# Kernel optimization log

Hardware: AMD Instinct MI355X
Metric: run time of the kernel (lower is better)

The kernel has to match this reference:

```python
import jax, jax.numpy as jnp
import numpy as np

N_NODES = 100000

def setup_inputs() -> dict:
    key = jax.random.key(0)
    ks = jax.random.split(key, 8)
    n_feat, nhid, nclass = 256, 128, 40
    n_edges = 1600000
    x = jax.random.normal(ks[0], (N_NODES, n_feat), dtype=jnp.float32)
    edge_index = jax.random.randint(ks[1], (2, n_edges), 0, N_NODES, dtype=jnp.int64)
    # Glorot-ish scaled weights
    W1 = jax.random.normal(ks[2], (n_feat, nhid), dtype=jnp.float32) / np.sqrt(n_feat)
    b1 = jnp.zeros((nhid,), dtype=jnp.float32)
    W2 = jax.random.normal(ks[3], (nhid, nhid), dtype=jnp.float32) / np.sqrt(nhid)
    b2 = jnp.zeros((nhid,), dtype=jnp.float32)
    Wc = jax.random.normal(ks[4], (nhid, nclass), dtype=jnp.float32) / np.sqrt(nhid)
    bc = jnp.zeros((nclass,), dtype=jnp.float32)
    return {"x": x, "edge_index": edge_index, "W1": W1, "b1": b1,
            "W2": W2, "b2": b2, "Wc": Wc, "bc": bc}


def _gcn_conv(x, src, dst, W, b, n_nodes):
    """PyG GCNConv: transform, then sym-normalized aggregation with self-loops.
    out_i = sum_{j in N(i) u {i}} (d_i^-1/2 d_j^-1/2) (x_j W) + b,
    where d = in-degree over A + I.
    """
    h = x @ W  # [N, out]
    ones = jnp.ones_like(dst, dtype=h.dtype)
    deg = jax.ops.segment_sum(ones, dst, num_segments=n_nodes) + 1.0  # + self loop
    dinv = jax.lax.rsqrt(deg)  # deg >= 1, always valid
    norm = dinv[src] * dinv[dst]  # [E]
    msg = h[src] * norm[:, None]  # [E, out]  (dominant gather traffic)
    agg = jax.ops.segment_sum(msg, dst, num_segments=n_nodes)
    agg = agg + h * (dinv * dinv)[:, None]  # self-loop contribution
    return agg + b


def reference(x, edge_index, W1, b1, W2, b2, Wc, bc):
    # eval mode: dropout is identity
    src, dst = edge_index[0], edge_index[1]
    n = x.shape[0]
    h = jax.nn.relu(_gcn_conv(x, src, dst, W1, b1, n))
    h = jax.nn.relu(_gcn_conv(h, src, dst, W2, b2, n))
    return h @ Wc + bc
```

## Files before the change

kernel.cpp:

```cpp
#include <hip/hip_runtime.h>
#include <hip/hip_bf16.h>
#include <hip/hip_fp16.h>
#include <type_traits>


typedef _Float16 half8 __attribute__((ext_vector_type(8)));
typedef float floatx4 __attribute__((ext_vector_type(4)));

#define EPB 8192


__device__ inline int block_incl_scan_256(int t, int* tmp) {
    int tid = threadIdx.x;
    tmp[tid] = t;
    __syncthreads();
    #pragma unroll
    for (int off = 1; off < 256; off <<= 1) {
        int v = (tid >= off) ? tmp[tid - off] : 0;
        __syncthreads();
        tmp[tid] += v;
        __syncthreads();
    }
    return tmp[tid];
}

template <int ITEMS>
__global__ __launch_bounds__(256) void k_scan1(const int* __restrict__ v,
                                               int* __restrict__ bsum, int n) {
    __shared__ int tmp[256];
    int base = blockIdx.x * (256 * ITEMS) + threadIdx.x * ITEMS;
    int t = 0;
    #pragma unroll
    for (int l = 0; l < ITEMS; ++l) {
        int i = base + l;
        t += (i < n) ? v[i] : 0;
    }
    block_incl_scan_256(t, tmp);
    if (threadIdx.x == 0) bsum[blockIdx.x] = tmp[255];
}

__global__ __launch_bounds__(256) void k_scan2(int* __restrict__ bsum, int nb) {
    __shared__ int tmp[256];
    int tid = threadIdx.x;
    int v = (tid < nb) ? bsum[tid] : 0;
    block_incl_scan_256(v, tmp);
    if (tid < nb) bsum[tid] = tid ? tmp[tid - 1] : 0;
}

template <int ITEMS>
__global__ __launch_bounds__(256) void k_scan3(const int* __restrict__ vin,
                                               const int* __restrict__ bsum,
                                               int* __restrict__ rp, int n) {
    __shared__ int tmp[256];
    int base = blockIdx.x * (256 * ITEMS) + threadIdx.x * ITEMS;
    int v[ITEMS];
    int t = 0;
    #pragma unroll
    for (int l = 0; l < ITEMS; ++l) {
        int i = base + l;
        v[l] = (i < n) ? vin[i] : 0;
        t += v[l];
    }
    block_incl_scan_256(t, tmp);
    int run = bsum[blockIdx.x] + (threadIdx.x ? tmp[threadIdx.x - 1] : 0);
    #pragma unroll
    for (int l = 0; l < ITEMS; ++l) {
        int i = base + l;
        if (i < n) rp[i] = run;
        run += v[l];
    }
}


__global__ __launch_bounds__(256) void k_histA(const int* __restrict__ dst,
                                               int* __restrict__ histM,
                                               int E, int nblk) {
    __shared__ int h[512];
    int tid = threadIdx.x;
    for (int i = tid; i < 512; i += 256) h[i] = 0;
    __syncthreads();
    int base = blockIdx.x * EPB;
    #pragma unroll 4
    for (int l = 0; l < EPB / 256; ++l) {
        int i = base + l * 256 + tid;
        if (i < E) atomicAdd(&h[dst[i] >> 8], 1);
    }
    __syncthreads();
    for (int i = tid; i < 512; i += 256)
        histM[i * nblk + blockIdx.x] = h[i];
}

__global__ __launch_bounds__(256) void k_scatterA(const int* __restrict__ src,
                                                  const int* __restrict__ dst,
                                                  const int* __restrict__ histS,
                                                  unsigned long long* __restrict__ eB,
                                                  int E, int nblk) {
    __shared__ int bse[512];
    __shared__ int cnt[512];
    int tid = threadIdx.x;
    for (int i = tid; i < 512; i += 256) {
        bse[i] = histS[i * nblk + blockIdx.x];
        cnt[i] = 0;
    }
    __syncthreads();
    int base = blockIdx.x * EPB;
    #pragma unroll 4
    for (int l = 0; l < EPB / 256; ++l) {
        int i = base + l * 256 + tid;
        if (i < E) {
            int d = dst[i];
            int s = src[i];
            int b = d >> 8;
            int r = atomicAdd(&cnt[b], 1);
            eB[bse[b] + r] = ((unsigned long long)(unsigned)d << 32) | (unsigned)s;
        }
    }
}

#define BCAP 4608
__global__ __launch_bounds__(256) void k_sortB(const unsigned long long* __restrict__ eB,
                                               const int* __restrict__ histS,
                                               int* __restrict__ srcS,
                                               int* __restrict__ rowptr,
                                               float* __restrict__ dinv,
                                               int n, int E, int nblk) {
    const int b   = blockIdx.x;
    const int tid = threadIdx.x;
    const int ni0 = b << 8;
    int s0 = histS[b * nblk];
    int s1 = (b < 511) ? histS[(b + 1) * nblk] : E;
    int cnt = s1 - s0;
    if (cnt > BCAP) cnt = BCAP;
    if (cnt == 0 && ni0 > n) return;

    __shared__ int hist[256];
    __shared__ int tmp[256];
    __shared__ int baseA[256];
    __shared__ int cntA[256];
    __shared__ int dstL[BCAP];
    __shared__ unsigned srcL[BCAP];
    __shared__ int lbA[256];

    hist[tid] = 0;
    cntA[tid] = 0;
    __syncthreads();
    for (int i = s0 + tid; i < s0 + cnt; i += 256) {
        int d = (int)(eB[i] >> 32);
        atomicAdd(&hist[d & 255], 1);
    }
    __syncthreads();
    int own  = hist[tid];
    int incl = block_incl_scan_256(own, tmp);
    baseA[tid] = incl - own;
    __syncthreads();
    for (int i = s0 + tid; i < s0 + cnt; i += 256) {
        unsigned long long v = eB[i];
        int d = (int)(v >> 32);
        int dig = d & 255;
        int r = atomicAdd(&cntA[dig], 1);
        int pos = baseA[dig] + r;
        dstL[pos] = d;
        srcL[pos] = (unsigned)v;
    }
    __syncthreads();
    for (int j = tid; j < cnt; j += 256)
        srcS[s0 + j] = (int)srcL[j];
    if (ni0 <= n) {
        int i = ni0 + tid;
        int lo = 0, hi = cnt;
        while (lo < hi) {
            int mid = (lo + hi) >> 1;
            if (dstL[mid] < i) lo = mid + 1; else hi = mid;
        }
        lbA[tid] = lo;
        __syncthreads();
        if (i <= n) {
            rowptr[i] = s0 + lo;
            if (i < n) {
                int ub = (tid < 255) ? lbA[tid + 1] : cnt;
                dinv[i] = rsqrtf((float)(ub - lo + 1));
            }
        }
    }
}

__global__ __launch_bounds__(256) void k_wcast_all(const float* __restrict__ W1,
                                                   _Float16* __restrict__ W1t,
                                                   const float* __restrict__ W2,
                                                   _Float16* __restrict__ W2t,
                                                   const float* __restrict__ Wc,
                                                   _Float16* __restrict__ Wct) {
    int i = blockIdx.x * 256 + threadIdx.x;
    if (i < 32768) {
        int c = i >> 8, k = i & 255;
        W1t[i] = (_Float16)W1[(size_t)k * 128 + c];
    } else if (i < 32768 + 16384) {
        int j = i - 32768;
        int c = j >> 7, k = j & 127;
        W2t[j] = (_Float16)W2[(size_t)k * 128 + c];
    } else if (i < 32768 + 16384 + 6144) {
        int j = i - 32768 - 16384;
        int c = j >> 7, k = j & 127;
        Wct[j] = (c < 40) ? (_Float16)Wc[(size_t)k * 40 + c] : (_Float16)0.f;
    }
}


template <int K, int BN, typename AT, typename OT>
__global__ __launch_bounds__(256) void gemm_pf(const AT* __restrict__ A,
                                               const _Float16* __restrict__ Wt,
                                               const float* __restrict__ bias,
                                               OT* __restrict__ C,
                                               int M, int N) {
    constexpr int KP = K + 8;
    constexpr int NT = BN / 16;
    constexpr int KS = K / 32;
    __shared__ __align__(16) _Float16 Bs[BN * KP];

    const int tid  = threadIdx.x;
    const int lane = tid & 63;
    const int wv   = tid >> 6;
    const int qd   = lane >> 4;
    const int ln15 = lane & 15;
    const int bm   = blockIdx.x * 64;

    int row  = bm + wv * 16 + ln15;
    int rowc = (row < M) ? row : (M - 1);

    float4 af[std::is_same<AT, float>::value ? KS : 1][2];
    half8  ah[std::is_same<AT, float>::value ? 1 : KS];
    if constexpr (std::is_same<AT, float>::value) {
        const float* p = A + (size_t)rowc * K + qd * 8;
        #pragma unroll
        for (int ks = 0; ks < KS; ++ks) {
            af[ks][0] = *(const float4*)(p + ks * 32);
            af[ks][1] = *(const float4*)(p + ks * 32 + 4);
        }
    } else {
        const _Float16* p = (const _Float16*)A + (size_t)rowc * K + qd * 8;
        #pragma unroll
        for (int ks = 0; ks < KS; ++ks)
            ah[ks] = *(const half8*)(p + ks * 32);
    }

    constexpr int TOT = BN * K / 8;
    #pragma unroll
    for (int i = 0; i < TOT / 256; ++i) {
        int idx = (i * 256 + tid) * 8;
        int col = idx / K;
        int kk  = idx % K;
        *(uint4*)&Bs[col * KP + kk] = *(const uint4*)(Wt + idx);
    }
    __syncthreads();

    floatx4 acc[NT];
    #pragma unroll
    for (int c = 0; c < NT; ++c) acc[c] = (floatx4){0.f, 0.f, 0.f, 0.f};

    #pragma unroll
    for (int ks = 0; ks < KS; ++ks) {
        half8 a;
        if constexpr (std::is_same<AT, float>::value) {
            float4 v0 = af[ks][0];
            float4 v1 = af[ks][1];
            a[0] = (_Float16)v0.x; a[1] = (_Float16)v0.y;
            a[2] = (_Float16)v0.z; a[3] = (_Float16)v0.w;
            a[4] = (_Float16)v1.x; a[5] = (_Float16)v1.y;
            a[6] = (_Float16)v1.z; a[7] = (_Float16)v1.w;
        } else {
            a = ah[ks];
        }
        #pragma unroll
        for (int c = 0; c < NT; ++c) {
            half8 b = *(const half8*)&Bs[(c * 16 + ln15) * KP + ks * 32 + qd * 8];
            acc[c] = __builtin_amdgcn_mfma_f32_16x16x32_f16(a, b, acc[c], 0, 0, 0);
        }
    }

    int baseRow = bm + wv * 16 + qd * 4;
    #pragma unroll
    for (int c = 0; c < NT; ++c) {
        int col = c * 16 + ln15;
        if constexpr (std::is_same<OT, _Float16>::value) {
            #pragma unroll
            for (int r = 0; r < 4; ++r) {
                int rr = baseRow + r;
                if (rr < M) C[(size_t)rr * N + col] = (_Float16)acc[c][r];
            }
        } else {
            float bv = (col < N && bias) ? bias[col] : 0.f;
            #pragma unroll
            for (int r = 0; r < 4; ++r) {
                int rr = baseRow + r;
                if (rr < M && col < N)
                    ((float*)C)[(size_t)rr * N + col] = acc[c][r] + bv;
            }
        }
    }
}


static __device__ __forceinline__ float2 h2f2u(unsigned int raw) {
    __half2 h = *(__half2*)&raw;
    return __half22float2(h);
}

__global__ __launch_bounds__(256) void gcn_agg(const unsigned int* __restrict__ h,
                                               const int* __restrict__ rowptr,
                                               const int* __restrict__ srcS,
                                               const float* __restrict__ dinv,
                                               const float* __restrict__ bias,
                                               unsigned int* __restrict__ out,
                                               int n, int do_relu) {
    int node = blockIdx.x * 4 + (threadIdx.x >> 6);
    if (node >= n) return;
    const int lane = threadIdx.x & 63;
    const int g    = lane >> 4;
    const int t    = lane & 15;

    const _Float16* hb = (const _Float16*)h;

    float di = dinv[node];
    int e0 = rowptr[node];
    int e1 = rowptr[node + 1];

    half8 sv = *(const half8*)(hb + (size_t)(unsigned)node * 128 + t * 8);
    const float4* b4 = (const float4*)bias;
    float4 blo = b4[t * 2 + 0];
    float4 bhi = b4[t * 2 + 1];

    float2 acc[4];
    #pragma unroll
    for (int i = 0; i < 4; ++i) acc[i] = make_float2(0.f, 0.f);

    for (int ce = e0; ce < e1; ce += 64) {
        int cnt = e1 - ce;
        cnt = (cnt < 64) ? cnt : 64;
        int colv = 0, wval = 0;
        if (lane < cnt) {
            int c = srcS[ce + lane];
            colv = c;
            wval = __float_as_int(di * dinv[c]);
        }
        #pragma unroll 2
        for (int d = 0; d < cnt; d += 4) {
            int idx = (d + g) << 2;
            int c   = __builtin_amdgcn_ds_bpermute(idx, colv);
            float w = __int_as_float(__builtin_amdgcn_ds_bpermute(idx, wval));
            const unsigned* hp = (const unsigned*)(hb + (size_t)(unsigned)c * 128 + t * 8);
            uint4 hv = *(const uint4*)hp;
            float2 u0 = h2f2u(hv.x);
            float2 u1 = h2f2u(hv.y);
            float2 u2 = h2f2u(hv.z);
            float2 u3 = h2f2u(hv.w);
            acc[0].x += u0.x * w; acc[0].y += u0.y * w;
            acc[1].x += u1.x * w; acc[1].y += u1.y * w;
            acc[2].x += u2.x * w; acc[2].y += u2.y * w;
            acc[3].x += u3.x * w; acc[3].y += u3.y * w;
        }
    }

    #pragma unroll
    for (int i = 0; i < 4; ++i) {
        acc[i].x += __shfl_xor(acc[i].x, 16);
        acc[i].y += __shfl_xor(acc[i].y, 16);
        acc[i].x += __shfl_xor(acc[i].x, 32);
        acc[i].y += __shfl_xor(acc[i].y, 32);
    }

    float s = di * di;
    float bb[8] = {blo.x, blo.y, blo.z, blo.w, bhi.x, bhi.y, bhi.z, bhi.w};
    half8 o;
    #pragma unroll
    for (int i = 0; i < 8; ++i) {
        float v = ((i & 1) ? acc[i >> 1].y : acc[i >> 1].x) + (float)sv[i] * s + bb[i];
        if (do_relu) v = fmaxf(v, 0.f);
        o[i] = (_Float16)v;
    }
    if (g == 0)
        *(half8*)((_Float16*)out + (size_t)(unsigned)node * 128 + t * 8) = o;
}


extern "C" void kernel_launch(void* const* d_in, const int* in_sizes, int n_in,
                              void* d_out, int out_size, void* d_ws, size_t ws_size,
                              hipStream_t stream) {
    const float* x  = (const float*)d_in[0];
    const int* eidx = (const int*)d_in[1];
    const float* W1 = (const float*)d_in[2];
    const float* b1 = (const float*)d_in[3];
    const float* W2 = (const float*)d_in[4];
    const float* b2 = (const float*)d_in[5];
    const float* Wc = (const float*)d_in[6];
    const float* bc = (const float*)d_in[7];
    float* out = (float*)d_out;

    const int NF = 256, NH = 128, NC = 40;
    const int n = in_sizes[0] / NF;
    const int E = in_sizes[1] / 2;
    const int* src = eidx;
    const int* dst = eidx + E;

    const int nblk = (E + EPB - 1) / EPB;
    const int hm   = 512 * nblk;
    const int nbA  = (hm + 4095) / 4096;

    char* wsb = (char*)d_ws;
    size_t off = 0;
    auto alloc = [&](size_t bytes) {
        char* p = wsb + off;
        off = (off + bytes + 511) & ~(size_t)511;
        return p;
    };
    _Float16* hbuf = (_Float16*)alloc((size_t)n * NH * 2);
    _Float16* abuf = (_Float16*)alloc((size_t)n * NH * 2);
    _Float16* W1t  = (_Float16*)alloc((size_t)128 * 256 * 2);
    _Float16* W2t  = (_Float16*)alloc((size_t)128 * 128 * 2);
    _Float16* Wct  = (_Float16*)alloc((size_t)48 * 128 * 2);
    unsigned long long* eB = (unsigned long long*)alloc((size_t)E * 8);
    int* srcS      = (int*)alloc((size_t)E * 4);
    int* histM     = (int*)alloc((size_t)hm * 4);
    int* histS     = (int*)alloc((size_t)hm * 4);
    int* rowptr    = (int*)alloc((size_t)(n + 1) * 4);
    float* dinv    = (float*)alloc((size_t)n * 4);
    int* bsumA     = (int*)alloc(1024);

    k_histA<<<nblk, 256, 0, stream>>>(dst, histM, E, nblk);
    k_scan1<16><<<nbA, 256, 0, stream>>>(histM, bsumA, hm);
    k_scan2<<<1, 256, 0, stream>>>(bsumA, nbA);
    k_scan3<16><<<nbA, 256, 0, stream>>>(histM, bsumA, histS, hm);
    k_scatterA<<<nblk, 256, 0, stream>>>(src, dst, histS, eB, E, nblk);
    k_sortB<<<512, 256, 0, stream>>>(eB, histS, srcS, rowptr, dinv, n, E, nblk);

    k_wcast_all<<<(32768 + 16384 + 6144 + 255) / 256, 256, 0, stream>>>(
        W1, W1t, W2, W2t, Wc, Wct);

    const int gB = (n + 63) / 64;
    gemm_pf<256, 128, float, _Float16><<<gB, 256, 0, stream>>>(x, W1t, nullptr, hbuf, n, NH);
    gcn_agg<<<(n + 3) / 4, 256, 0, stream>>>((const unsigned int*)hbuf, rowptr, srcS, dinv, b1,
                                             (unsigned int*)abuf, n, 1);
    gemm_pf<128, 128, _Float16, _Float16><<<gB, 256, 0, stream>>>(abuf, W2t, nullptr, hbuf, n, NH);
    gcn_agg<<<(n + 3) / 4, 256, 0, stream>>>((const unsigned int*)hbuf, rowptr, srcS, dinv, b2,
                                             (unsigned int*)abuf, n, 1);
    gemm_pf<128, 48, _Float16, float><<<gB, 256, 0, stream>>>(abuf, Wct, bc, out, n, NC);
}
```

Baseline: 394.8 us.

## Split edge buffer into packed src/dst-low arrays, chunk GEMM K, nontemporal agg I/O

The intermediate edge bucket buffer moves from 8-byte packed (dst,src) pairs to a 4-byte src array plus a 1-byte low-digit dst array. This cuts scatter and sort traffic, and sortB now keeps short digits in shared memory and compares them against tid. The GEMM loads weights into LDS in K chunks of 128, which halves LDS use for the K=256 layer and may improve occupancy, at the cost of an extra barrier. The aggregation kernel uses nontemporal loads for srcS and nontemporal stores for its output.

Measured after the change: 425.5 us. 1.08x slower.

```diff
diff --git a/kernel.cpp b/kernel.cpp
--- a/kernel.cpp
+++ b/kernel.cpp
@@ -6,6 +6,7 @@
 
 typedef _Float16 half8 __attribute__((ext_vector_type(8)));
 typedef float floatx4 __attribute__((ext_vector_type(4)));
+typedef unsigned int uint4v __attribute__((ext_vector_type(4)));
 
 #define EPB 8192
 
@@ -93,7 +94,8 @@
 __global__ __launch_bounds__(256) void k_scatterA(const int* __restrict__ src,
                                                   const int* __restrict__ dst,
                                                   const int* __restrict__ histS,
-                                                  unsigned long long* __restrict__ eB,
+                                                  unsigned int* __restrict__ srcB,
+                                                  unsigned char* __restrict__ dstB,
                                                   int E, int nblk) {
     __shared__ int bse[512];
     __shared__ int cnt[512];
@@ -112,13 +114,16 @@
             int s = src[i];
             int b = d >> 8;
             int r = atomicAdd(&cnt[b], 1);
-            eB[bse[b] + r] = ((unsigned long long)(unsigned)d << 32) | (unsigned)s;
+            int pos = bse[b] + r;
+            srcB[pos] = (unsigned)s;
+            dstB[pos] = (unsigned char)(d & 255);
         }
     }
 }
 
 #define BCAP 4608
-__global__ __launch_bounds__(256) void k_sortB(const unsigned long long* __restrict__ eB,
+__global__ __launch_bounds__(256) void k_sortB(const unsigned int* __restrict__ srcB,
+                                               const unsigned char* __restrict__ dstB,
                                                const int* __restrict__ histS,
                                                int* __restrict__ srcS,
                                                int* __restrict__ rowptr,
@@ -137,30 +142,27 @@
     __shared__ int tmp[256];
     __shared__ int baseA[256];
     __shared__ int cntA[256];
-    __shared__ int dstL[BCAP];
+    __shared__ short dstL[BCAP];
     __shared__ unsigned srcL[BCAP];
     __shared__ int lbA[256];
 
     hist[tid] = 0;
     cntA[tid] = 0;
     __syncthreads();
-    for (int i = s0 + tid; i < s0 + cnt; i += 256) {
-        int d = (int)(eB[i] >> 32);
-        atomicAdd(&hist[d & 255], 1);
-    }
+    for (int i = s0 + tid; i < s0 + cnt; i += 256)
+        atomicAdd(&hist[dstB[i]], 1);
     __syncthreads();
     int own  = hist[tid];
     int incl = block_incl_scan_256(own, tmp);
     baseA[tid] = incl - own;
     __syncthreads();
     for (int i = s0 + tid; i < s0 + cnt; i += 256) {
-        unsigned long long v = eB[i];
-        int d = (int)(v >> 32);
-        int dig = d & 255;
+        int dig = dstB[i];
+        unsigned s = srcB[i];
         int r = atomicAdd(&cntA[dig], 1);
         int pos = baseA[dig] + r;
-        dstL[pos] = d;
-        srcL[pos] = (unsigned)v;
+        dstL[pos] = (short)dig;
+        srcL[pos] = s;
     }
     __syncthreads();
     for (int j = tid; j < cnt; j += 256)
@@ -170,7 +172,7 @@
         int lo = 0, hi = cnt;
         while (lo < hi) {
             int mid = (lo + hi) >> 1;
-            if (dstL[mid] < i) lo = mid + 1; else hi = mid;
+            if ((int)dstL[mid] < tid) lo = mid + 1; else hi = mid;
         }
         lbA[tid] = lo;
         __syncthreads();
@@ -212,7 +214,8 @@
                                                const float* __restrict__ bias,
                                                OT* __restrict__ C,
                                                int M, int N) {
-    constexpr int KP = K + 8;
+    constexpr int KC = (K > 128) ? 128 : K;
+    constexpr int KP = KC + 8;
     constexpr int NT = BN / 16;
     constexpr int KS = K / 32;
     __shared__ __align__(16) _Float16 Bs[BN * KP];
@@ -243,37 +246,43 @@
             ah[ks] = *(const half8*)(p + ks * 32);
     }
 
-    constexpr int TOT = BN * K / 8;
-    #pragma unroll
-    for (int i = 0; i < TOT / 256; ++i) {
-        int idx = (i * 256 + tid) * 8;
-        int col = idx / K;
-        int kk  = idx % K;
-        *(uint4*)&Bs[col * KP + kk] = *(const uint4*)(Wt + idx);
-    }
-    __syncthreads();
-
     floatx4 acc[NT];
     #pragma unroll
     for (int c = 0; c < NT; ++c) acc[c] = (floatx4){0.f, 0.f, 0.f, 0.f};
 
     #pragma unroll
-    for (int ks = 0; ks < KS; ++ks) {
-        half8 a;
-        if constexpr (std::is_same<AT, float>::value) {
-            float4 v0 = af[ks][0];
-            float4 v1 = af[ks][1];
-            a[0] = (_Float16)v0.x; a[1] = (_Float16)v0.y;
-            a[2] = (_Float16)v0.z; a[3] = (_Float16)v0.w;
-            a[4] = (_Float16)v1.x; a[5] = (_Float16)v1.y;
-            a[6] = (_Float16)v1.z; a[7] = (_Float16)v1.w;
-        } else {
-            a = ah[ks];
-        }
+    for (int kh = 0; kh < K; kh += KC) {
+        if (kh) __syncthreads();
+        constexpr int TOT = BN * KC / 8;
         #pragma unroll
-        for (int c = 0; c < NT; ++c) {
-            half8 b = *(const half8*)&Bs[(c * 16 + ln15) * KP + ks * 32 + qd * 8];
-            acc[c] = __builtin_amdgcn_mfma_f32_16x16x32_f16(a, b, acc[c], 0, 0, 0);
+        for (int i = 0; i < TOT / 256; ++i) {
+            int idx = (i * 256 + tid) * 8;
+            int col = idx / KC;
+            int kk  = idx % KC;
+            *(uint4*)&Bs[col * KP + kk] =
+                *(const uint4*)(Wt + (size_t)col * K + kh + kk);
+        }
+        __syncthreads();
+
+        #pragma unroll
+        for (int ks2 = 0; ks2 < KC / 32; ++ks2) {
+            const int ks = kh / 32 + ks2;
+            half8 a;
+            if constexpr (std::is_same<AT, float>::value) {
+                float4 v0 = af[ks][0];
+                float4 v1 = af[ks][1];
+                a[0] = (_Float16)v0.x; a[1] = (_Float16)v0.y;
+                a[2] = (_Float16)v0.z; a[3] = (_Float16)v0.w;
+                a[4] = (_Float16)v1.x; a[5] = (_Float16)v1.y;
+                a[6] = (_Float16)v1.z; a[7] = (_Float16)v1.w;
+            } else {
+                a = ah[ks];
+            }
+            #pragma unroll
+            for (int c = 0; c < NT; ++c) {
+                half8 b = *(const half8*)&Bs[(c * 16 + ln15) * KP + ks2 * 32 + qd * 8];
+                acc[c] = __builtin_amdgcn_mfma_f32_16x16x32_f16(a, b, acc[c], 0, 0, 0);
+            }
         }
     }
 
@@ -338,7 +347,7 @@
         cnt = (cnt < 64) ? cnt : 64;
         int colv = 0, wval = 0;
         if (lane < cnt) {
-            int c = srcS[ce + lane];
+            int c = __builtin_nontemporal_load(srcS + ce + lane);
             colv = c;
             wval = __float_as_int(di * dinv[c]);
         }
@@ -377,8 +386,10 @@
         if (do_relu) v = fmaxf(v, 0.f);
         o[i] = (_Float16)v;
     }
-    if (g == 0)
-        *(half8*)((_Float16*)out + (size_t)(unsigned)node * 128 + t * 8) = o;
+    if (g == 0) {
+        uint4v* dstp = (uint4v*)((_Float16*)out + (size_t)(unsigned)node * 128 + t * 8);
+        __builtin_nontemporal_store(*(uint4v*)&o, dstp);
+    }
 }
 
 
@@ -417,7 +428,8 @@
     _Float16* W1t  = (_Float16*)alloc((size_t)128 * 256 * 2);
     _Float16* W2t  = (_Float16*)alloc((size_t)128 * 128 * 2);
     _Float16* Wct  = (_Float16*)alloc((size_t)48 * 128 * 2);
-    unsigned long long* eB = (unsigned long long*)alloc((size_t)E * 8);
+    unsigned int* srcB  = (unsigned int*)alloc((size_t)E * 4);
+    unsigned char* dstB = (unsigned char*)alloc((size_t)E);
     int* srcS      = (int*)alloc((size_t)E * 4);
     int* histM     = (int*)alloc((size_t)hm * 4);
     int* histS     = (int*)alloc((size_t)hm * 4);
@@ -429,8 +441,8 @@
     k_scan1<16><<<nbA, 256, 0, stream>>>(histM, bsumA, hm);
     k_scan2<<<1, 256, 0, stream>>>(bsumA, nbA);
     k_scan3<16><<<nbA, 256, 0, stream>>>(histM, bsumA, histS, hm);
-    k_scatterA<<<nblk, 256, 0, stream>>>(src, dst, histS, eB, E, nblk);
-    k_sortB<<<512, 256, 0, stream>>>(eB, histS, srcS, rowptr, dinv, n, E, nblk);
+    k_scatterA<<<nblk, 256, 0, stream>>>(src, dst, histS, srcB, dstB, E, nblk);
+    k_sortB<<<512, 256, 0, stream>>>(srcB, dstB, histS, srcS, rowptr, dinv, n, E, nblk);
 
     k_wcast_all<<<(32768 + 16384 + 6144 + 255) / 256, 256, 0, stream>>>(
         W1, W1t, W2, W2t, Wc, Wct);
```
